# Performance work log

Measured on AMD Instinct MI355X. Metric: run time of the kernel, lower is better.

## Reference

```python
import jax, jax.numpy as jnp
import numpy as np

FL = 320       # frame length
FS = 80        # frame shift
ORDER = 16     # poly order (a[0] == 1)
EMPH = 0.97    # pre/de-emphasis coefficient


def setup_inputs() -> dict:
    key = jax.random.key(0)
    k1, k2 = jax.random.split(key)
    B, F = 64, 3000
    L = F * FS  # 240000
    excit = jax.random.normal(k1, (B, L, 1), dtype=jnp.float32) * 0.1
    # LPC coefficients: a[0] = 1, remaining taps small for numerical stability
    rest = jax.random.normal(k2, (B, F, ORDER - 1), dtype=jnp.float32) * (0.3 / (ORDER - 1))
    lpc_coef = jnp.concatenate([jnp.ones((B, F, 1), jnp.float32), rest], axis=-1)
    return {"excit": excit, "lpc_coef": lpc_coef}


def reference(excit, lpc_coef):
    """LPCSynthesisPytorch: AR synthesis recursion followed by de-emphasis.

    excit:    (B, L, 1)
    lpc_coef: (B, F, order), a[0] assumed 1, L = F * FS
    returns:  (B, L, 1)
    """
    B, L, _ = excit.shape
    order = lpc_coef.shape[-1]

    # Per-sample AR taps a[1:], expanded frame->sample, time-major for scan.
    a = jnp.repeat(lpc_coef[:, :, 1:], FS, axis=1)[:, :L]      # (B, L, order-1)
    a_t = jnp.transpose(a, (1, 0, 2))                          # (L, B, order-1)
    e_t = jnp.transpose(excit[..., 0], (1, 0))                 # (L, B)

    def ar_step(buf, inp):
        # buf: (B, order-1) = [x[n-order+1], ..., x[n-1]] (last entry most recent)
        a_n, e_n = inp
        # predicted = sum_k a[k] * x[n-k]; output = excit - predicted
        pre = -jnp.sum(a_n * buf[:, ::-1], axis=-1)
        out = e_n + pre
        buf = jnp.concatenate([buf[:, 1:], out[:, None]], axis=-1)
        return buf, out

    buf0 = jnp.zeros((B, order - 1), dtype=excit.dtype)
    _, y_t = jax.lax.scan(ar_step, buf0, (a_t, e_t))           # (L, B)

    # De-emphasis IIR: z[n] = y[n] + EMPH * z[n-1], z[-1] = 0
    def deemph_step(prev, x):
        cur = x + EMPH * prev
        return cur, cur

    _, z_t = jax.lax.scan(deemph_step, jnp.zeros((B,), excit.dtype), y_t)
    return jnp.transpose(z_t, (1, 0))[..., None]               # (B, L, 1)
```

## Files before the change

kernel.cpp:

```cpp
#include <hip/hip_runtime.h>


namespace {
constexpr int kHS = 40;
constexpr int kF = 3000;
constexpr int kH = 2 * kF;
constexpr int kL = kHS * kH;
constexpr int kL4 = kL / 4;
constexpr int kOrder = 16;
constexpr int kB = 64;
constexpr float kEmph = 0.97f;
constexpr int kThreads = 64;
constexpr int kJunk = 9;
constexpr int kEmitH = kThreads - kJunk;
constexpr int kInSlots = kThreads + 2;
constexpr int kIn4 = kInSlots * 10;
constexpr int kSlotW = 44;
constexpr int kCols = (kH + kEmitH - 1) / kEmitH;
constexpr float kLg97 = -4.3943347e-2f;
constexpr float kR1 = 0.2957118f;
constexpr float kR2 = 0.08744547f;
constexpr float kR3 = 0.02585867f;
constexpr float kR4 = 0.00764671f;
constexpr float kR5 = 0.00226126f;
constexpr float kR6 = 6.6867e-4f;
constexpr float kR7 = 1.9773e-4f;
constexpr float kR8 = 5.8472e-5f;

typedef float vfloat4 __attribute__((ext_vector_type(4)));
}

#define AR_SAMPLE(A, s, e_in, ACC)                                         \
  float ACC;                                                               \
  {                                                                        \
    float t0 = (e_in);                                                     \
    t0 = fmaf(-A[14], x[((s)-15) & 15], t0);                               \
    t0 = fmaf(-A[13], x[((s)-14) & 15], t0);                               \
    t0 = fmaf(-A[12], x[((s)-13) & 15], t0);                               \
    t0 = fmaf(-A[11], x[((s)-12) & 15], t0);                               \
    t0 = fmaf(-A[10], x[((s)-11) & 15], t0);                               \
    float t1 = -A[9] * x[((s)-10) & 15];                                   \
    t1 = fmaf(-A[8], x[((s)-9) & 15], t1);                                 \
    t1 = fmaf(-A[7], x[((s)-8) & 15], t1);                                 \
    t1 = fmaf(-A[6], x[((s)-7) & 15], t1);                                 \
    t1 = fmaf(-A[5], x[((s)-6) & 15], t1);                                 \
    float t2 = -A[4] * x[((s)-5) & 15];                                    \
    t2 = fmaf(-A[3], x[((s)-4) & 15], t2);                                 \
    t2 = fmaf(-A[2], x[((s)-3) & 15], t2);                                 \
    t2 = fmaf(-A[1], x[((s)-2) & 15], t2);                                 \
    const float t01 = t0 + t1;                      \
    t2 = fmaf(-A[0], x[((s)-1) & 15], t2);            \
    ACC = t01 + t2;                                           \
    x[(s)&15] = ACC;                                                       \
  }

__global__ __launch_bounds__(kThreads) void lpc_synth_kernel(
    const float* __restrict__ excit, const float* __restrict__ coef,
    float* __restrict__ out) {
  __shared__ float s_x[kInSlots * kSlotW];
  __shared__ float s_zend[kThreads];
  __shared__ float s_zp[kEmitH];

  const int tid = threadIdx.x;
  const int b = blockIdx.y;
  const int hbase = blockIdx.x * kEmitH;
  const int ht = hbase + tid - kJunk;
  const int hc = min(max(ht, 0), kH - 1);
  const int hw = min(max(ht - 2, 0), kH - 1);

  const float* __restrict__ ebase = excit + (size_t)b * kL;
  const float* __restrict__ cbase = coef + (size_t)b * kF * kOrder;

  {
    const vfloat4* __restrict__ eg = (const vfloat4*)ebase;
    const int base4 = (hbase - 11) * 10;
#pragma unroll
    for (int p = 0; p < 10; ++p) {
      const int i = tid + p * kThreads;
      const int g4 = min(max(base4 + i, 0), kL4 - 1);
      const vfloat4 v = eg[g4];
      const int slot = i / 10;
      const int o = i - slot * 10;
      *(vfloat4*)(s_x + slot * kSlotW + o * 4) = v;
    }
    if (tid < kIn4 - 10 * kThreads) {
      const int i = 10 * kThreads + tid;
      const int g4 = min(max(base4 + i, 0), kL4 - 1);
      const vfloat4 v = eg[g4];
      const int slot = i / 10;
      const int o = i - slot * 10;
      *(vfloat4*)(s_x + slot * kSlotW + o * 4) = v;
    }
  }

  const vfloat4* __restrict__ cp_ =
      (const vfloat4*)(cbase + (size_t)(hw >> 1) * kOrder);
  const vfloat4* __restrict__ cc_ =
      (const vfloat4*)(cbase + (size_t)(hc >> 1) * kOrder);
  const vfloat4 p0 = cp_[0], p1 = cp_[1], p2 = cp_[2], p3 = cp_[3];
  const vfloat4 q0 = cc_[0], q1 = cc_[1], q2 = cc_[2], q3 = cc_[3];

  __syncthreads();

  float pa_[15] = {p0.y, p0.z, p0.w, p1.x, p1.y, p1.z, p1.w, p2.x,
                   p2.y, p2.z, p2.w, p3.x, p3.y, p3.z, p3.w};
  const float ca_[15] = {q0.y, q0.z, q0.w, q1.x, q1.y, q1.z, q1.w, q2.x,
                         q2.y, q2.z, q2.w, q3.x, q3.y, q3.z, q3.w};

  float x[16];
#pragma unroll
  for (int i = 0; i < 16; ++i) x[i] = 0.f;

  {
    const float* __restrict__ s2 = s_x + tid * kSlotW;
    const float* __restrict__ s1 = s_x + (tid + 1) * kSlotW;
    const float m2 = (ht >= 2) ? 1.f : 0.f;
    const float m1 = (ht >= 1) ? 1.f : 0.f;
#pragma unroll
    for (int j = 8; j < 10; ++j) {
      const vfloat4 v = *(const vfloat4*)(s2 + 4 * j);
      const float f_[4] = {m2 * v.x, m2 * v.y, m2 * v.z, m2 * v.w};
#pragma unroll
      for (int q = 0; q < 4; ++q) {
        AR_SAMPLE(pa_, 4 * (j - 8) + q, f_[q], acc)
        (void)acc;
      }
    }
    if (ht & 1) {
#pragma unroll
      for (int k = 0; k < 15; ++k) pa_[k] = ca_[k];
    }
#pragma unroll
    for (int j = 0; j < 10; ++j) {
      const vfloat4 v = *(const vfloat4*)(s1 + 4 * j);
      const float f_[4] = {m1 * v.x, m1 * v.y, m1 * v.z, m1 * v.w};
#pragma unroll
      for (int q = 0; q < 4; ++q) {
        AR_SAMPLE(pa_, 8 + 4 * j + q, f_[q], acc)
        (void)acc;
      }
    }
  }
  __syncthreads();

  float z = 0.f;
  {
    float* __restrict__ so = s_x + (tid + 2) * kSlotW;
#pragma unroll
    for (int j = 0; j < 10; ++j) {
      const vfloat4 v = *(const vfloat4*)(so + 4 * j);
      vfloat4 zv;
#pragma unroll
      for (int q = 0; q < 4; ++q) {
        AR_SAMPLE(ca_, 48 + 4 * j + q, v[q], acc)
        z = fmaf(kEmph, z, acc);
        if (q == 0) zv.x = z;
        if (q == 1) zv.y = z;
        if (q == 2) zv.z = z;
        if (q == 3) zv.w = z;
      }
      *(vfloat4*)(so + 4 * j) = zv;
    }
  }
  s_zend[tid] = (ht < 0 || ht >= kH) ? 0.f : z;
  __syncthreads();

  if (tid < kEmitH) {
    float Zp = s_zend[tid + 8];
    Zp = fmaf(kR1, s_zend[tid + 7], Zp);
    Zp = fmaf(kR2, s_zend[tid + 6], Zp);
    Zp = fmaf(kR3, s_zend[tid + 5], Zp);
    Zp = fmaf(kR4, s_zend[tid + 4], Zp);
    Zp = fmaf(kR5, s_zend[tid + 3], Zp);
    Zp = fmaf(kR6, s_zend[tid + 2], Zp);
    Zp = fmaf(kR7, s_zend[tid + 1], Zp);
    Zp = fmaf(kR8, s_zend[tid + 0], Zp);
    s_zp[tid] = Zp;
  }
  __syncthreads();

  {
    const int nv4 = min(kEmitH, kH - hbase) * 10;
    vfloat4* __restrict__ ob =
        (vfloat4*)(out + (size_t)b * kL + (size_t)hbase * kHS);
#pragma unroll 1
    for (int i = tid; i < nv4; i += kThreads) {
      const int k = i / 10;
      const int j = i - 10 * k;
      const vfloat4 h =
          *(const vfloat4*)(s_x + (k + 11) * kSlotW + 4 * j);
      const float Zp = s_zp[k];
      const float ee = __builtin_exp2f(kLg97 * (float)(4 * j + 1));
      vfloat4 v;
      v.x = fmaf(ee, Zp, h.x);
      v.y = fmaf(ee * 0.97f, Zp, h.y);
      v.z = fmaf(ee * 0.9409f, Zp, h.z);
      v.w = fmaf(ee * 0.912673f, Zp, h.w);
      ob[i] = v;
    }
  }
}
#undef AR_SAMPLE

extern "C" void kernel_launch(void* const* d_in, const int* in_sizes, int n_in,
                              void* d_out, int out_size, void* d_ws,
                              size_t ws_size, hipStream_t stream) {
  const float* excit = (const float*)d_in[0];
  const float* coef = (const float*)d_in[1];
  float* out = (float*)d_out;

  dim3 grid(kCols, kB);
  lpc_synth_kernel<<<grid, kThreads, 0, stream>>>(excit, coef, out);
}
```

Before: 126.3 us.

## Process two tiles per block with register-prefetched excitation and wave-level LDS fences

Each 64-thread block now handles two consecutive tiles. The next tile's excitation is prefetched into registers while the current tile is computed, and __syncthreads is replaced with an s_waitcnt lgkmcnt(0) fence, which is enough because the block is a single wavefront. Launch bounds now request 3 waves per SIMD, and the grid width is hardcoded to 55 columns. The aim is to hide global load latency and cut barrier overhead, at the cost of extra registers for the prefetch buffer and half as many blocks.

```diff
diff --git a/kernel.cpp b/kernel.cpp
--- a/kernel.cpp
+++ b/kernel.cpp
@@ -15,8 +15,10 @@
 constexpr int kEmitH = kThreads - kJunk;
 constexpr int kInSlots = kThreads + 2;
 constexpr int kIn4 = kInSlots * 10;
+constexpr int kTail = kIn4 - 10 * kThreads;
 constexpr int kSlotW = 44;
-constexpr int kCols = (kH + kEmitH - 1) / kEmitH;
+constexpr int kNT = 2;
+constexpr int kCols = 55;
 constexpr float kLg97 = -4.3943347e-2f;
 constexpr float kR1 = 0.2957118f;
 constexpr float kR2 = 0.08744547f;
@@ -28,6 +30,12 @@
 constexpr float kR8 = 5.8472e-5f;
 
 typedef float vfloat4 __attribute__((ext_vector_type(4)));
+
+__device__ __forceinline__ void lds_fence() {
+  __builtin_amdgcn_sched_barrier(0);
+  asm volatile("s_waitcnt lgkmcnt(0)" ::: "memory");
+  __builtin_amdgcn_sched_barrier(0);
+}
 }
 
 #define AR_SAMPLE(A, s, e_in, ACC)                                         \
@@ -54,7 +62,17 @@
     x[(s)&15] = ACC;                                                       \
   }
 
-__global__ __launch_bounds__(kThreads) void lpc_synth_kernel(
+#define LOAD_TILE(TILE)                                                    \
+  {                                                                        \
+    const int base4_ = ((TILE)*kEmitH - 11) * 10;                          \
+    _Pragma("unroll") for (int p = 0; p < 11; ++p) {                       \
+      const int i_ = min(tid + p * kThreads, kIn4 - 1);                    \
+      const int g4_ = min(max(base4_ + i_, 0), kL4 - 1);                   \
+      ex[p] = eg[g4_];                                                     \
+    }                                                                      \
+  }
+
+__global__ __launch_bounds__(kThreads, 3) void lpc_synth_kernel(
     const float* __restrict__ excit, const float* __restrict__ coef,
     float* __restrict__ out) {
   __shared__ float s_x[kInSlots * kSlotW];
@@ -63,144 +81,146 @@
 
   const int tid = threadIdx.x;
   const int b = blockIdx.y;
-  const int hbase = blockIdx.x * kEmitH;
-  const int ht = hbase + tid - kJunk;
-  const int hc = min(max(ht, 0), kH - 1);
-  const int hw = min(max(ht - 2, 0), kH - 1);
+  const int tile0 = blockIdx.x * kNT;
 
   const float* __restrict__ ebase = excit + (size_t)b * kL;
   const float* __restrict__ cbase = coef + (size_t)b * kF * kOrder;
-
-  {
-    const vfloat4* __restrict__ eg = (const vfloat4*)ebase;
-    const int base4 = (hbase - 11) * 10;
-#pragma unroll
-    for (int p = 0; p < 10; ++p) {
-      const int i = tid + p * kThreads;
-      const int g4 = min(max(base4 + i, 0), kL4 - 1);
-      const vfloat4 v = eg[g4];
-      const int slot = i / 10;
-      const int o = i - slot * 10;
-      *(vfloat4*)(s_x + slot * kSlotW + o * 4) = v;
-    }
-    if (tid < kIn4 - 10 * kThreads) {
-      const int i = 10 * kThreads + tid;
-      const int g4 = min(max(base4 + i, 0), kL4 - 1);
-      const vfloat4 v = eg[g4];
-      const int slot = i / 10;
-      const int o = i - slot * 10;
-      *(vfloat4*)(s_x + slot * kSlotW + o * 4) = v;
-    }
+  const vfloat4* __restrict__ eg = (const vfloat4*)ebase;
+
+  vfloat4 ex[11];
+
+  LOAD_TILE(tile0)
+
+#pragma unroll
+  for (int t = 0; t < kNT; ++t) {
+    const int tile = tile0 + t;
+    const int hbase = tile * kEmitH;
+    const int ht = hbase + tid - kJunk;
+    const int hc = min(max(ht, 0), kH - 1);
+    const int hw = min(max(ht - 2, 0), kH - 1);
+
+#pragma unroll
+    for (int p = 0; p < 11; ++p) {
+      if (p < 10 || tid < kTail) {
+        const int i = tid + p * kThreads;
+        const int slot = i / 10;
+        const int o = i - slot * 10;
+        *(vfloat4*)(s_x + slot * kSlotW + o * 4) = ex[p];
+      }
+    }
+
+    const vfloat4* __restrict__ cp_ =
+        (const vfloat4*)(cbase + (size_t)(hw >> 1) * kOrder);
+    const vfloat4* __restrict__ cc_ =
+        (const vfloat4*)(cbase + (size_t)(hc >> 1) * kOrder);
+    const vfloat4 p0 = cp_[0], p1 = cp_[1], p2 = cp_[2], p3 = cp_[3];
+    const vfloat4 q0 = cc_[0], q1 = cc_[1], q2 = cc_[2], q3 = cc_[3];
+    if (t + 1 < kNT) LOAD_TILE(tile0 + t + 1)
+
+    lds_fence();
+
+    float pa_[15] = {p0.y, p0.z, p0.w, p1.x, p1.y, p1.z, p1.w, p2.x,
+                     p2.y, p2.z, p2.w, p3.x, p3.y, p3.z, p3.w};
+    const float ca_[15] = {q0.y, q0.z, q0.w, q1.x, q1.y, q1.z, q1.w, q2.x,
+                           q2.y, q2.z, q2.w, q3.x, q3.y, q3.z, q3.w};
+
+    float x[16];
+#pragma unroll
+    for (int i = 0; i < 16; ++i) x[i] = 0.f;
+
+    {
+      const float* __restrict__ s2 = s_x + tid * kSlotW;
+      const float* __restrict__ s1 = s_x + (tid + 1) * kSlotW;
+      const float m2 = (ht >= 2) ? 1.f : 0.f;
+      const float m1 = (ht >= 1) ? 1.f : 0.f;
+#pragma unroll
+      for (int j = 8; j < 10; ++j) {
+        const vfloat4 v = *(const vfloat4*)(s2 + 4 * j);
+        const float f_[4] = {m2 * v.x, m2 * v.y, m2 * v.z, m2 * v.w};
+#pragma unroll
+        for (int q = 0; q < 4; ++q) {
+          AR_SAMPLE(pa_, 4 * (j - 8) + q, f_[q], acc)
+          (void)acc;
+        }
+      }
+      if (ht & 1) {
+#pragma unroll
+        for (int k = 0; k < 15; ++k) pa_[k] = ca_[k];
+      }
+#pragma unroll
+      for (int j = 0; j < 10; ++j) {
+        const vfloat4 v = *(const vfloat4*)(s1 + 4 * j);
+        const float f_[4] = {m1 * v.x, m1 * v.y, m1 * v.z, m1 * v.w};
+#pragma unroll
+        for (int q = 0; q < 4; ++q) {
+          AR_SAMPLE(pa_, 8 + 4 * j + q, f_[q], acc)
+          (void)acc;
+        }
+      }
+    }
+    lds_fence();
+
+    float z = 0.f;
+    {
+      float* __restrict__ so = s_x + (tid + 2) * kSlotW;
+#pragma unroll
+      for (int j = 0; j < 10; ++j) {
+        const vfloat4 v = *(const vfloat4*)(so + 4 * j);
+        vfloat4 zv;
+#pragma unroll
+        for (int q = 0; q < 4; ++q) {
+          AR_SAMPLE(ca_, 48 + 4 * j + q, v[q], acc)
+          z = fmaf(kEmph, z, acc);
+          if (q == 0) zv.x = z;
+          if (q == 1) zv.y = z;
+          if (q == 2) zv.z = z;
+          if (q == 3) zv.w = z;
+        }
+        *(vfloat4*)(so + 4 * j) = zv;
+      }
+    }
+    s_zend[tid] = (ht < 0 || ht >= kH) ? 0.f : z;
+    lds_fence();
+
+    if (tid < kEmitH) {
+      float Zp = s_zend[tid + 8];
+      Zp = fmaf(kR1, s_zend[tid + 7], Zp);
+      Zp = fmaf(kR2, s_zend[tid + 6], Zp);
+      Zp = fmaf(kR3, s_zend[tid + 5], Zp);
+      Zp = fmaf(kR4, s_zend[tid + 4], Zp);
+      Zp = fmaf(kR5, s_zend[tid + 3], Zp);
+      Zp = fmaf(kR6, s_zend[tid + 2], Zp);
+      Zp = fmaf(kR7, s_zend[tid + 1], Zp);
+      Zp = fmaf(kR8, s_zend[tid + 0], Zp);
+      s_zp[tid] = Zp;
+    }
+    lds_fence();
+
+    {
+      const int nv4 = min(kEmitH, kH - hbase) * 10;
+      vfloat4* __restrict__ ob =
+          (vfloat4*)(out + (size_t)b * kL + (size_t)hbase * kHS);
+#pragma unroll 1
+      for (int i = tid; i < nv4; i += kThreads) {
+        const int k = i / 10;
+        const int j = i - 10 * k;
+        const vfloat4 h =
+            *(const vfloat4*)(s_x + (k + 11) * kSlotW + 4 * j);
+        const float Zp = s_zp[k];
+        const float ee = __builtin_exp2f(kLg97 * (float)(4 * j + 1));
+        vfloat4 v;
+        v.x = fmaf(ee, Zp, h.x);
+        v.y = fmaf(ee * 0.97f, Zp, h.y);
+        v.z = fmaf(ee * 0.9409f, Zp, h.z);
+        v.w = fmaf(ee * 0.912673f, Zp, h.w);
+        ob[i] = v;
+      }
+    }
+    lds_fence();
   }
-
-  const vfloat4* __restrict__ cp_ =
-      (const vfloat4*)(cbase + (size_t)(hw >> 1) * kOrder);
-  const vfloat4* __restrict__ cc_ =
-      (const vfloat4*)(cbase + (size_t)(hc >> 1) * kOrder);
-  const vfloat4 p0 = cp_[0], p1 = cp_[1], p2 = cp_[2], p3 = cp_[3];
-  const vfloat4 q0 = cc_[0], q1 = cc_[1], q2 = cc_[2], q3 = cc_[3];
-
-  __syncthreads();
-
-  float pa_[15] = {p0.y, p0.z, p0.w, p1.x, p1.y, p1.z, p1.w, p2.x,
-                   p2.y, p2.z, p2.w, p3.x, p3.y, p3.z, p3.w};
-  const float ca_[15] = {q0.y, q0.z, q0.w, q1.x, q1.y, q1.z, q1.w, q2.x,
-                         q2.y, q2.z, q2.w, q3.x, q3.y, q3.z, q3.w};
-
-  float x[16];
-#pragma unroll
-  for (int i = 0; i < 16; ++i) x[i] = 0.f;
-
-  {
-    const float* __restrict__ s2 = s_x + tid * kSlotW;
-    const float* __restrict__ s1 = s_x + (tid + 1) * kSlotW;
-    const float m2 = (ht >= 2) ? 1.f : 0.f;
-    const float m1 = (ht >= 1) ? 1.f : 0.f;
-#pragma unroll
-    for (int j = 8; j < 10; ++j) {
-      const vfloat4 v = *(const vfloat4*)(s2 + 4 * j);
-      const float f_[4] = {m2 * v.x, m2 * v.y, m2 * v.z, m2 * v.w};
-#pragma unroll
-      for (int q = 0; q < 4; ++q) {
-        AR_SAMPLE(pa_, 4 * (j - 8) + q, f_[q], acc)
-        (void)acc;
-      }
-    }
-    if (ht & 1) {
-#pragma unroll
-      for (int k = 0; k < 15; ++k) pa_[k] = ca_[k];
-    }
-#pragma unroll
-    for (int j = 0; j < 10; ++j) {
-      const vfloat4 v = *(const vfloat4*)(s1 + 4 * j);
-      const float f_[4] = {m1 * v.x, m1 * v.y, m1 * v.z, m1 * v.w};
-#pragma unroll
-      for (int q = 0; q < 4; ++q) {
-        AR_SAMPLE(pa_, 8 + 4 * j + q, f_[q], acc)
-        (void)acc;
-      }
-    }
-  }
-  __syncthreads();
-
-  float z = 0.f;
-  {
-    float* __restrict__ so = s_x + (tid + 2) * kSlotW;
-#pragma unroll
-    for (int j = 0; j < 10; ++j) {
-      const vfloat4 v = *(const vfloat4*)(so + 4 * j);
-      vfloat4 zv;
-#pragma unroll
-      for (int q = 0; q < 4; ++q) {
-        AR_SAMPLE(ca_, 48 + 4 * j + q, v[q], acc)
-        z = fmaf(kEmph, z, acc);
-        if (q == 0) zv.x = z;
-        if (q == 1) zv.y = z;
-        if (q == 2) zv.z = z;
-        if (q == 3) zv.w = z;
-      }
-      *(vfloat4*)(so + 4 * j) = zv;
-    }
-  }
-  s_zend[tid] = (ht < 0 || ht >= kH) ? 0.f : z;
-  __syncthreads();
-
-  if (tid < kEmitH) {
-    float Zp = s_zend[tid + 8];
-    Zp = fmaf(kR1, s_zend[tid + 7], Zp);
-    Zp = fmaf(kR2, s_zend[tid + 6], Zp);
-    Zp = fmaf(kR3, s_zend[tid + 5], Zp);
-    Zp = fmaf(kR4, s_zend[tid + 4], Zp);
-    Zp = fmaf(kR5, s_zend[tid + 3], Zp);
-    Zp = fmaf(kR6, s_zend[tid + 2], Zp);
-    Zp = fmaf(kR7, s_zend[tid + 1], Zp);
-    Zp = fmaf(kR8, s_zend[tid + 0], Zp);
-    s_zp[tid] = Zp;
-  }
-  __syncthreads();
-
-  {
-    const int nv4 = min(kEmitH, kH - hbase) * 10;
-    vfloat4* __restrict__ ob =
-        (vfloat4*)(out + (size_t)b * kL + (size_t)hbase * kHS);
-#pragma unroll 1
-    for (int i = tid; i < nv4; i += kThreads) {
-      const int k = i / 10;
-      const int j = i - 10 * k;
-      const vfloat4 h =
-          *(const vfloat4*)(s_x + (k + 11) * kSlotW + 4 * j);
-      const float Zp = s_zp[k];
-      const float ee = __builtin_exp2f(kLg97 * (float)(4 * j + 1));
-      vfloat4 v;
-      v.x = fmaf(ee, Zp, h.x);
-      v.y = fmaf(ee * 0.97f, Zp, h.y);
-      v.z = fmaf(ee * 0.9409f, Zp, h.z);
-      v.w = fmaf(ee * 0.912673f, Zp, h.w);
-      ob[i] = v;
-    }
-  }
 }
 #undef AR_SAMPLE
+#undef LOAD_TILE
 
 extern "C" void kernel_launch(void* const* d_in, const int* in_sizes, int n_in,
                               void* d_out, int out_size, void* d_ws,
```

New measurement: 137.9 us. 9.2% more time.
